# Performance work log

Hardware: AMD Instinct MI355X
Metric: run time of the kernel (lower is better)

The kernel has to match this reference:

```python
import jax, jax.numpy as jnp
import numpy as np

B, N, D, H = 2, 512, 64, 128  # batch, tokens, feature dim, hidden (=2*D)
OUT = 64


def setup_inputs() -> dict:
    key = jax.random.key(0)
    ks = jax.random.split(key, 11)
    sH = 1.0 / np.sqrt(H)
    inp = {
        "x": jax.random.normal(ks[0], (B, N, D), dtype=jnp.float32),
        # inner MLP: Linear(2D->H), ReLU, Linear(H->H), ReLU, Linear(H->H)
        "W1": jax.random.normal(ks[1], (2 * D, H), dtype=jnp.float32) / np.sqrt(2 * D),
        "b1": jnp.zeros((H,), jnp.float32),
        "W2": jax.random.normal(ks[2], (H, H), dtype=jnp.float32) * sH,
        "b2": jnp.zeros((H,), jnp.float32),
        "W3": jax.random.normal(ks[3], (H, H), dtype=jnp.float32) * sH,
        "b3": jnp.zeros((H,), jnp.float32),
        # outer MLP: Linear(H->H), ReLU, Linear(H->OUT)
        "V1": jax.random.normal(ks[4], (H, H), dtype=jnp.float32) * sH,
        "c1": jnp.zeros((H,), jnp.float32),
        "V2": jax.random.normal(ks[5], (H, OUT), dtype=jnp.float32) * sH,
        "c2": jnp.zeros((OUT,), jnp.float32),
    }
    return inp


def reference(x, W1, b1, W2, b2, W3, b3, V1, c1, V2, c2):
    d = x.shape[-1]
    # pair[b,i,j] = cat(x[b,j], x[b,i]); fuse cat with first linear:
    # pair @ W1 = x[b,j] @ W1[:d] + x[b,i] @ W1[d:]
    xa = jnp.einsum('bnd,dh->bnh', x, W1[:d])   # contribution of pair_a (index j)
    xb = jnp.einsum('bnd,dh->bnh', x, W1[d:])   # contribution of pair_b (index i)
    h = jax.nn.relu(xa[:, None, :, :] + xb[:, :, None, :] + b1)  # [B,N,N,H]
    h = jax.nn.relu(jnp.einsum('bijh,hk->bijk', h, W2) + b2)
    rel = jnp.einsum('bijh,hk->bijk', h, W3) + b3                # inner output [B,N,N,H]
    pooled = rel.sum(axis=(1, 2))                                # [B,H]
    o = jax.nn.relu(pooled @ V1 + c1)
    return o @ V2 + c2                                           # [B,OUT]
```

## Files before the change

kernel.cpp:

```cpp
#include <hip/hip_runtime.h>
#include <hip/hip_bf16.h>

#define B_ 2
#define N_ 512
#define D_ 64
#define H_ 128
#define OUT_ 64
#define NPAIRS_F 262144.0f

using bf16x8 = __attribute__((ext_vector_type(8))) __bf16;
using f32x4  = __attribute__((ext_vector_type(4))) float;
using f32x2  = __attribute__((ext_vector_type(2))) float;


__global__ __launch_bounds__(256) void prep_kernel(
    const float* __restrict__ x, const float* __restrict__ W1,
    const float* __restrict__ b1, const float* __restrict__ W2,
    float* __restrict__ xa, float* __restrict__ xb,
    __hip_bfloat16* __restrict__ w2t, float* __restrict__ S)
{
    int idx = blockIdx.x * 256 + threadIdx.x;
    if (idx < B_ * N_ * H_) {
        int h  = idx & (H_ - 1);
        int bn = idx >> 7;
        const float* xr = x + bn * D_;
        float aa = 0.f, ab = 0.f;
        #pragma unroll
        for (int k = 0; k < D_; k++) {
            float xv = xr[k];
            aa += xv * W1[k * H_ + h];
            ab += xv * W1[(k + D_) * H_ + h];
        }
        xa[idx] = aa + b1[h];
        xb[idx] = ab;
    }
    if (idx < H_ * H_) {
        int k = idx & (H_ - 1);
        int n = idx >> 7;
        w2t[n * H_ + k] = __float2bfloat16(W2[k * H_ + n]);
    }
    if (idx < B_ * H_) S[idx] = 0.f;
}

__global__ __launch_bounds__(256, 2) void pair_kernel(
    const float* __restrict__ xa, const float* __restrict__ xb,
    const uint4* __restrict__ w2t, const float* __restrict__ b2,
    float* __restrict__ S)
{
    const int tid  = threadIdx.x;
    const int lane = tid & 63;
    const int wid  = tid >> 6;
    const int l15  = lane & 15;
    const int quad = lane >> 4;

    const int j0 = blockIdx.x * 16;
    const int i0 = blockIdx.y * 64;
    const int b  = blockIdx.z;

    __shared__ float xbs[64 * H_];

    const f32x4* xbsrc = (const f32x4*)(xb + ((size_t)(b * N_) + i0) * H_);
    f32x4 stmp[8];
    #pragma unroll
    for (int t = 0; t < 8; t++) stmp[t] = xbsrc[t * 256 + tid];

    bf16x8 bfrag[8][4];
    #pragma unroll
    for (int c = 0; c < 8; c++) {
        int row = 16 * c + l15;
        #pragma unroll
        for (int s = 0; s < 4; s++) {
            union { uint4 u; bf16x8 v; } cv;
            cv.u = w2t[row * 16 + s * 4 + quad];
            bfrag[c][s] = cv.v;
        }
    }

    const float* xaB = xa + (size_t)(b * N_ + j0 + l15) * H_;
    f32x4 av[4][2];
    #pragma unroll
    for (int s = 0; s < 4; s++) {
        const f32x4* p = (const f32x4*)(xaB + s * 32 + quad * 8);
        av[s][0] = p[0];
        av[s][1] = p[1];
    }

    float nb2[8];
    #pragma unroll
    for (int c = 0; c < 8; c++) nb2[c] = -b2[16 * c + l15];

    {
        f32x4* dst = (f32x4*)xbs;
        #pragma unroll
        for (int t = 0; t < 8; t++) dst[t * 256 + tid] = stmp[t];
    }
    __syncthreads();

    f32x2 csum[8];
    #pragma unroll
    for (int c = 0; c < 8; c++) { csum[c][0] = 0.f; csum[c][1] = 0.f; }

    const f32x4 zero4 = {0.f, 0.f, 0.f, 0.f};
    const float* xrow = xbs + (wid * 16) * H_;

    #pragma unroll 2
    for (int r = 0; r < 16; r++) {
        const float* xr = xrow + r * H_;

        bf16x8 afr[4];
        #pragma unroll
        for (int s = 0; s < 4; s++) {
            const f32x4* p = (const f32x4*)(xr + s * 32 + quad * 8);
            f32x4 f0 = av[s][0] + p[0];
            f32x4 f1 = av[s][1] + p[1];
            f0 = __builtin_elementwise_max(f0, zero4);
            f1 = __builtin_elementwise_max(f1, zero4);
            bf16x8 a;
            #pragma unroll
            for (int t = 0; t < 4; t++) {
                a[t]     = (__bf16)f0[t];
                a[t + 4] = (__bf16)f1[t];
            }
            afr[s] = a;
        }

        #pragma unroll
        for (int c = 0; c < 8; c++) {
            f32x4 acc = {0.f, 0.f, 0.f, 0.f};
            #pragma unroll
            for (int s = 0; s < 4; s++)
                acc = __builtin_amdgcn_mfma_f32_16x16x32_bf16(afr[s], bfrag[c][s], acc, 0, 0, 0);
            f32x2 lo; lo[0] = acc[0]; lo[1] = acc[1];
            f32x2 hi; hi[0] = acc[2]; hi[1] = acc[3];
            f32x2 nb; nb[0] = nb2[c]; nb[1] = nb2[c];
            lo = __builtin_elementwise_max(lo, nb);
            hi = __builtin_elementwise_max(hi, nb);
            csum[c] += lo + hi;
        }
    }

    float redv[8];
    #pragma unroll
    for (int c = 0; c < 8; c++) {
        float v = csum[c][0] + csum[c][1];
        v += __shfl_xor(v, 16, 64);
        v += __shfl_xor(v, 32, 64);
        redv[c] = v;
    }

    __shared__ float sred[4][H_];
    if (lane < 16) {
        #pragma unroll
        for (int c = 0; c < 8; c++) sred[wid][c * 16 + l15] = redv[c];
    }
    __syncthreads();
    if (tid < H_) {
        float tot = sred[0][tid] + sred[1][tid] + sred[2][tid] + sred[3][tid];
        atomicAdd(&S[b * H_ + tid], tot);
    }
}

__global__ __launch_bounds__(128) void tail_kernel(
    const float* __restrict__ S, const float* __restrict__ b2,
    const float* __restrict__ W3, const float* __restrict__ b3,
    const float* __restrict__ V1, const float* __restrict__ c1,
    const float* __restrict__ V2, const float* __restrict__ c2,
    float* __restrict__ out)
{
    __shared__ float Ss[H_], pool[H_], ov[H_];
    const int b = blockIdx.x, t = threadIdx.x;
    Ss[t] = S[b * H_ + t] + NPAIRS_F * b2[t];
    __syncthreads();
    float acc = 0.f;
    for (int k = 0; k < H_; k++) acc += Ss[k] * W3[k * H_ + t];
    pool[t] = acc + NPAIRS_F * b3[t];
    __syncthreads();
    acc = c1[t];
    for (int k = 0; k < H_; k++) acc += pool[k] * V1[k * H_ + t];
    ov[t] = acc > 0.f ? acc : 0.f;
    __syncthreads();
    if (t < OUT_) {
        acc = c2[t];
        for (int k = 0; k < H_; k++) acc += ov[k] * V2[k * OUT_ + t];
        out[b * OUT_ + t] = acc;
    }
}

extern "C" void kernel_launch(void* const* d_in, const int* in_sizes, int n_in,
                              void* d_out, int out_size, void* d_ws, size_t ws_size,
                              hipStream_t stream) {
    const float* x  = (const float*)d_in[0];
    const float* W1 = (const float*)d_in[1];
    const float* b1 = (const float*)d_in[2];
    const float* W2 = (const float*)d_in[3];
    const float* b2 = (const float*)d_in[4];
    const float* W3 = (const float*)d_in[5];
    const float* b3 = (const float*)d_in[6];
    const float* V1 = (const float*)d_in[7];
    const float* c1 = (const float*)d_in[8];
    const float* V2 = (const float*)d_in[9];
    const float* c2 = (const float*)d_in[10];
    float* out = (float*)d_out;

    char* ws = (char*)d_ws;
    float*          xa  = (float*)(ws);
    float*          xb  = (float*)(ws + 524288);
    __hip_bfloat16* w2t = (__hip_bfloat16*)(ws + 1048576);
    float*          S   = (float*)(ws + 1048576 + 32768);

    prep_kernel<<<512, 256, 0, stream>>>(x, W1, b1, W2, xa, xb, w2t, S);
    dim3 g2(N_ / 16, N_ / 64, B_);
    pair_kernel<<<g2, 256, 0, stream>>>(xa, xb, (const uint4*)w2t, b2, S);
    tail_kernel<<<B_, 128, 0, stream>>>(S, b2, W3, b3, V1, c1, V2, c2, out);
}
```

Measured before the change: 117.0 us.

## Fuse first-layer projection and W2 conversion into pair kernel, drop atomics

Result: faster. 113.3 us (-3.2%).

```diff
diff --git a/kernel.cpp b/kernel.cpp
--- a/kernel.cpp
+++ b/kernel.cpp
@@ -13,39 +13,17 @@
 using f32x2  = __attribute__((ext_vector_type(2))) float;
 
 
-__global__ __launch_bounds__(256) void prep_kernel(
+__device__ __forceinline__ bf16x8 pack_bf16x8(f32x4 u0, f32x4 u1) {
+    bf16x8 a;
+    #pragma unroll
+    for (int t = 0; t < 4; t++) { a[t] = (__bf16)u0[t]; a[t + 4] = (__bf16)u1[t]; }
+    return a;
+}
+
+__global__ __launch_bounds__(256, 2) void pair_kernel(
     const float* __restrict__ x, const float* __restrict__ W1,
     const float* __restrict__ b1, const float* __restrict__ W2,
-    float* __restrict__ xa, float* __restrict__ xb,
-    __hip_bfloat16* __restrict__ w2t, float* __restrict__ S)
-{
-    int idx = blockIdx.x * 256 + threadIdx.x;
-    if (idx < B_ * N_ * H_) {
-        int h  = idx & (H_ - 1);
-        int bn = idx >> 7;
-        const float* xr = x + bn * D_;
-        float aa = 0.f, ab = 0.f;
-        #pragma unroll
-        for (int k = 0; k < D_; k++) {
-            float xv = xr[k];
-            aa += xv * W1[k * H_ + h];
-            ab += xv * W1[(k + D_) * H_ + h];
-        }
-        xa[idx] = aa + b1[h];
-        xb[idx] = ab;
-    }
-    if (idx < H_ * H_) {
-        int k = idx & (H_ - 1);
-        int n = idx >> 7;
-        w2t[n * H_ + k] = __float2bfloat16(W2[k * H_ + n]);
-    }
-    if (idx < B_ * H_) S[idx] = 0.f;
-}
-
-__global__ __launch_bounds__(256, 2) void pair_kernel(
-    const float* __restrict__ xa, const float* __restrict__ xb,
-    const uint4* __restrict__ w2t, const float* __restrict__ b2,
-    float* __restrict__ S)
+    const float* __restrict__ b2, float* __restrict__ P)
 {
     const int tid  = threadIdx.x;
     const int lane = tid & 63;
@@ -58,49 +36,108 @@
     const int b  = blockIdx.z;
 
     __shared__ float xbs[64 * H_];
-
-    const f32x4* xbsrc = (const f32x4*)(xb + ((size_t)(b * N_) + i0) * H_);
-    f32x4 stmp[8];
-    #pragma unroll
-    for (int t = 0; t < 8; t++) stmp[t] = xbsrc[t * 256 + tid];
+    __shared__ float xas[16 * 132];
+    __shared__ float sred[4][H_];
+
+    const f32x4 zero4 = {0.f, 0.f, 0.f, 0.f};
+
+    const float* xiB = x + ((size_t)(b * N_) + i0 + wid * 16 + l15) * D_;
+    const float* xjB = x + ((size_t)(b * N_) + j0 + l15) * D_;
+    bf16x8 Ai[2], Aj[2];
+    #pragma unroll
+    for (int s2 = 0; s2 < 2; s2++) {
+        const f32x4* pi = (const f32x4*)(xiB + s2 * 32 + quad * 8);
+        const f32x4* pj = (const f32x4*)(xjB + s2 * 32 + quad * 8);
+        Ai[s2] = pack_bf16x8(pi[0], pi[1]);
+        Aj[s2] = pack_bf16x8(pj[0], pj[1]);
+    }
+
+    bf16x8 Bb[8][2];
+    #pragma unroll
+    for (int ct = 0; ct < 8; ct++) {
+        #pragma unroll
+        for (int s2 = 0; s2 < 2; s2++) {
+            f32x4 u0, u1;
+            #pragma unroll
+            for (int t = 0; t < 4; t++) {
+                u0[t] = W1[(64 + s2 * 32 + quad * 8 + t) * H_ + ct * 16 + l15];
+                u1[t] = W1[(64 + s2 * 32 + quad * 8 + 4 + t) * H_ + ct * 16 + l15];
+            }
+            Bb[ct][s2] = pack_bf16x8(u0, u1);
+        }
+    }
+    bf16x8 Ba[2][2];
+    #pragma unroll
+    for (int e = 0; e < 2; e++) {
+        int ct = 2 * wid + e;
+        #pragma unroll
+        for (int s2 = 0; s2 < 2; s2++) {
+            f32x4 u0, u1;
+            #pragma unroll
+            for (int t = 0; t < 4; t++) {
+                u0[t] = W1[(s2 * 32 + quad * 8 + t) * H_ + ct * 16 + l15];
+                u1[t] = W1[(s2 * 32 + quad * 8 + 4 + t) * H_ + ct * 16 + l15];
+            }
+            Ba[e][s2] = pack_bf16x8(u0, u1);
+        }
+    }
+
+    #pragma unroll
+    for (int ct = 0; ct < 8; ct++) {
+        f32x4 acc = zero4;
+        acc = __builtin_amdgcn_mfma_f32_16x16x32_bf16(Ai[0], Bb[ct][0], acc, 0, 0, 0);
+        acc = __builtin_amdgcn_mfma_f32_16x16x32_bf16(Ai[1], Bb[ct][1], acc, 0, 0, 0);
+        #pragma unroll
+        for (int reg = 0; reg < 4; reg++)
+            xbs[(wid * 16 + quad * 4 + reg) * H_ + ct * 16 + l15] = acc[reg];
+    }
+    #pragma unroll
+    for (int e = 0; e < 2; e++) {
+        int ct = 2 * wid + e;
+        f32x4 acc = zero4;
+        acc = __builtin_amdgcn_mfma_f32_16x16x32_bf16(Aj[0], Ba[e][0], acc, 0, 0, 0);
+        acc = __builtin_amdgcn_mfma_f32_16x16x32_bf16(Aj[1], Ba[e][1], acc, 0, 0, 0);
+        float bv = b1[ct * 16 + l15];
+        #pragma unroll
+        for (int reg = 0; reg < 4; reg++)
+            xas[(quad * 4 + reg) * 132 + ct * 16 + l15] = acc[reg] + bv;
+    }
+
+    __builtin_amdgcn_sched_barrier(0);
 
     bf16x8 bfrag[8][4];
     #pragma unroll
     for (int c = 0; c < 8; c++) {
-        int row = 16 * c + l15;
         #pragma unroll
         for (int s = 0; s < 4; s++) {
-            union { uint4 u; bf16x8 v; } cv;
-            cv.u = w2t[row * 16 + s * 4 + quad];
-            bfrag[c][s] = cv.v;
-        }
-    }
-
-    const float* xaB = xa + (size_t)(b * N_ + j0 + l15) * H_;
+            f32x4 u0, u1;
+            #pragma unroll
+            for (int t = 0; t < 4; t++) {
+                u0[t] = W2[(s * 32 + quad * 8 + t) * H_ + c * 16 + l15];
+                u1[t] = W2[(s * 32 + quad * 8 + 4 + t) * H_ + c * 16 + l15];
+            }
+            bfrag[c][s] = pack_bf16x8(u0, u1);
+        }
+    }
+
+    float nb2[8];
+    #pragma unroll
+    for (int c = 0; c < 8; c++) nb2[c] = -b2[16 * c + l15];
+
+    __syncthreads();
+
     f32x4 av[4][2];
     #pragma unroll
     for (int s = 0; s < 4; s++) {
-        const f32x4* p = (const f32x4*)(xaB + s * 32 + quad * 8);
+        const f32x4* p = (const f32x4*)(xas + l15 * 132 + s * 32 + quad * 8);
         av[s][0] = p[0];
         av[s][1] = p[1];
     }
 
-    float nb2[8];
-    #pragma unroll
-    for (int c = 0; c < 8; c++) nb2[c] = -b2[16 * c + l15];
-
-    {
-        f32x4* dst = (f32x4*)xbs;
-        #pragma unroll
-        for (int t = 0; t < 8; t++) dst[t * 256 + tid] = stmp[t];
-    }
-    __syncthreads();
-
     f32x2 csum[8];
     #pragma unroll
     for (int c = 0; c < 8; c++) { csum[c][0] = 0.f; csum[c][1] = 0.f; }
 
-    const f32x4 zero4 = {0.f, 0.f, 0.f, 0.f};
     const float* xrow = xbs + (wid * 16) * H_;
 
     #pragma unroll 2
@@ -115,18 +152,12 @@
             f32x4 f1 = av[s][1] + p[1];
             f0 = __builtin_elementwise_max(f0, zero4);
             f1 = __builtin_elementwise_max(f1, zero4);
-            bf16x8 a;
-            #pragma unroll
-            for (int t = 0; t < 4; t++) {
-                a[t]     = (__bf16)f0[t];
-                a[t + 4] = (__bf16)f1[t];
-            }
-            afr[s] = a;
+            afr[s] = pack_bf16x8(f0, f1);
         }
 
         #pragma unroll
         for (int c = 0; c < 8; c++) {
-            f32x4 acc = {0.f, 0.f, 0.f, 0.f};
+            f32x4 acc = zero4;
             #pragma unroll
             for (int s = 0; s < 4; s++)
                 acc = __builtin_amdgcn_mfma_f32_16x16x32_bf16(afr[s], bfrag[c][s], acc, 0, 0, 0);
@@ -148,7 +179,6 @@
         redv[c] = v;
     }
 
-    __shared__ float sred[4][H_];
     if (lane < 16) {
         #pragma unroll
         for (int c = 0; c < 8; c++) sred[wid][c * 16 + l15] = redv[c];
@@ -156,12 +186,13 @@
     __syncthreads();
     if (tid < H_) {
         float tot = sred[0][tid] + sred[1][tid] + sred[2][tid] + sred[3][tid];
-        atomicAdd(&S[b * H_ + tid], tot);
+        int id = blockIdx.x * 8 + blockIdx.y;
+        P[((size_t)(b * H_ + tid)) * 256 + id] = tot;
     }
 }
 
 __global__ __launch_bounds__(128) void tail_kernel(
-    const float* __restrict__ S, const float* __restrict__ b2,
+    const float* __restrict__ P, const float* __restrict__ b2,
     const float* __restrict__ W3, const float* __restrict__ b3,
     const float* __restrict__ V1, const float* __restrict__ c1,
     const float* __restrict__ V2, const float* __restrict__ c2,
@@ -169,7 +200,11 @@
 {
     __shared__ float Ss[H_], pool[H_], ov[H_];
     const int b = blockIdx.x, t = threadIdx.x;
-    Ss[t] = S[b * H_ + t] + NPAIRS_F * b2[t];
+    const f32x4* Pr = (const f32x4*)(P + ((size_t)(b * H_ + t)) * 256);
+    f32x4 s4 = {0.f, 0.f, 0.f, 0.f};
+    #pragma unroll 8
+    for (int k = 0; k < 64; k++) s4 += Pr[k];
+    Ss[t] = (s4[0] + s4[1] + s4[2] + s4[3]) + NPAIRS_F * b2[t];
     __syncthreads();
     float acc = 0.f;
     for (int k = 0; k < H_; k++) acc += Ss[k] * W3[k * H_ + t];
@@ -202,14 +237,9 @@
     const float* c2 = (const float*)d_in[10];
     float* out = (float*)d_out;
 
-    char* ws = (char*)d_ws;
-    float*          xa  = (float*)(ws);
-    float*          xb  = (float*)(ws + 524288);
-    __hip_bfloat16* w2t = (__hip_bfloat16*)(ws + 1048576);
-    float*          S   = (float*)(ws + 1048576 + 32768);
-
-    prep_kernel<<<512, 256, 0, stream>>>(x, W1, b1, W2, xa, xb, w2t, S);
+    float* P = (float*)d_ws;
+
     dim3 g2(N_ / 16, N_ / 64, B_);
-    pair_kernel<<<g2, 256, 0, stream>>>(xa, xb, (const uint4*)w2t, b2, S);
-    tail_kernel<<<B_, 128, 0, stream>>>(S, b2, W3, b3, V1, c1, V2, c2, out);
-}
+    pair_kernel<<<g2, 256, 0, stream>>>(x, W1, b1, W2, b2, P);
+    tail_kernel<<<B_, 128, 0, stream>>>(P, b2, W3, b3, V1, c1, V2, c2, out);
+}
```
